# Performance work log

Hardware: AMD Instinct MI355X
Metric: run time of the kernel (lower is better)

## Reference

```python
import jax, jax.numpy as jnp
import numpy as np

NUM_GROUPS = 8   # num_groups1, recursive_index=False path
NUM_HEADS = 8


def setup_inputs() -> dict:
    key = jax.random.key(0)
    k1, k2, k3 = jax.random.split(key, 3)
    B, C, H, W = 4, 256, 64, 64
    x = jax.random.normal(k1, (B, C, H, W), dtype=jnp.float32)
    w_qkv = jax.random.normal(k2, (3 * C, C), dtype=jnp.float32) * 0.02
    w_proj = jax.random.normal(k3, (C, C), dtype=jnp.float32) * 0.02
    b_proj = jnp.zeros((C,), dtype=jnp.float32)
    return {"x": x, "w_qkv": w_qkv, "w_proj": w_proj, "b_proj": b_proj}


def reference(x, w_qkv, w_proj, b_proj):
    B, C, H, W = x.shape
    N = H * W
    G = NUM_GROUPS
    nh = NUM_HEADS
    hd = C // nh
    M = N // G
    scale = hd ** -0.5

    # b c h w -> b (h w) c
    xf = x.reshape(B, C, N).transpose(0, 2, 1)  # [B, N, C]

    # qkv linear (no bias), then split into groups / heads
    qkv = (xf @ w_qkv.T).reshape(B, G, M, 3, nh, hd)
    qkv = jnp.transpose(qkv, (3, 0, 1, 4, 2, 5))  # [3, B, G, nh, M, hd]
    q, k, v = qkv[0], qkv[1], qkv[2]

    # grouped multi-head attention, manual softmax
    attn = jax.nn.softmax(jnp.einsum('bghmd,bghnd->bghmn', q, k) * scale, axis=-1)
    out = jnp.einsum('bghmn,bghnd->bghmd', attn, v)

    # [B,G,nh,M,hd] -> [B,G,M,C] -> [B,N,C]
    out = out.transpose(0, 1, 3, 2, 4).reshape(B, N, C)

    out = out @ w_proj.T + b_proj

    # b (h w) c -> b c h w
    return out.transpose(0, 2, 1).reshape(B, C, H, W)
```

## Files before the change

### kernel.cpp

```cpp
#include <hip/hip_runtime.h>
#include <hip/hip_bf16.h>

#define Bb 4
#define Cc 256
#define Nn 4096
#define Gg 8
#define NHh 8
#define HDd 32
#define Mm 512

typedef __bf16 bf16_t;
typedef __bf16 bf16x2 __attribute__((ext_vector_type(2)));
typedef __bf16 bf16x4 __attribute__((ext_vector_type(4)));
typedef __bf16 bf16x8 __attribute__((ext_vector_type(8)));
typedef float f32x4 __attribute__((ext_vector_type(4)));

#define LSCALE (0.17677669529663687f * 1.44269504088896340f)

__device__ __forceinline__ void load_lds16(const bf16_t* g, bf16_t* l) {
  __builtin_amdgcn_global_load_lds(
      (const __attribute__((address_space(1))) void*)g,
      (__attribute__((address_space(3))) void*)l, 16, 0, 0);
}

__global__ __launch_bounds__(256) void prep_kernel(
    const float* __restrict__ x, bf16_t* __restrict__ xT,
    const float* __restrict__ wqkv, const float* __restrict__ wproj,
    bf16_t* __restrict__ wq_b, bf16_t* __restrict__ wp_b) {
  int bid = blockIdx.x, tid = threadIdx.x;
  if (bid >= 1024) {
    int i = (bid - 1024) * 256 + tid;
    wq_b[i] = (bf16_t)wqkv[i];
    if (i < Cc * Cc) wp_b[i] = (bf16_t)wproj[i];
    return;
  }
  __shared__ float t[64][65];
  int b = bid >> 8, c0 = ((bid >> 6) & 3) * 64, n0 = (bid & 63) * 64;
  const float* xp = x + ((long long)b * Cc + c0) * Nn + n0;
#pragma unroll
  for (int it = 0; it < 4; ++it) {
    int idx = it * 256 + tid;
    int r = idx >> 4, col = (idx & 15) * 4;
    f32x4 v = *(const f32x4*)&xp[(long long)r * Nn + col];
    t[r][col] = v[0];
    t[r][col + 1] = v[1];
    t[r][col + 2] = v[2];
    t[r][col + 3] = v[3];
  }
  __syncthreads();
  bf16_t* op = xT + ((long long)b * Nn + n0) * Cc + c0;
#pragma unroll
  for (int it = 0; it < 2; ++it) {
    int idx = it * 256 + tid;
    int n = idx >> 3, cg = (idx & 7) * 8;
    bf16x8 w;
#pragma unroll
    for (int j = 0; j < 8; ++j) w[j] = (bf16_t)t[cg + j][n];
    *(bf16x8*)&op[(long long)n * Cc + cg] = w;
  }
}

__global__ __launch_bounds__(256, 4) void qkv_gemm_kernel(
    const bf16_t* __restrict__ xT, const bf16_t* __restrict__ wqb,
    bf16_t* __restrict__ Qh, bf16_t* __restrict__ Kh, bf16_t* __restrict__ Vh) {
  __shared__ bf16_t smem[20480];
  int bid = blockIdx.x;
  int m0 = (bid / 3) * 64;
  int n0 = (bid % 3) * 256;
  int tid = threadIdx.x, lane = tid & 63, wid = tid >> 6;
  int quad = lane >> 4, l16 = lane & 15;
  int wn = wid * 64;

  f32x4 acc[4][4];
#pragma unroll
  for (int i = 0; i < 4; ++i)
#pragma unroll
    for (int j = 0; j < 4; ++j) acc[i][j] = (f32x4){0.f, 0.f, 0.f, 0.f};

  int scol = (lane & 3) * 8;
  int arow = lane >> 2;
  auto stage = [&](int bufi, int k0) {
    load_lds16(&xT[(long long)(m0 + wid * 16 + arow) * Cc + k0 + scol],
               &smem[bufi * 2048 + wid * 512]);
#pragma unroll
    for (int r = 0; r < 4; ++r) {
      int ch = wid * 4 + r;
      load_lds16(&wqb[(long long)(n0 + ch * 16 + arow) * Cc + k0 + scol],
                 &smem[4096 + bufi * 8192 + ch * 512]);
    }
  };

  stage(0, 0);
  __syncthreads();
  for (int t = 0; t < 8; ++t) {
    if (t < 7) stage((t + 1) & 1, (t + 1) * 32);
    const bf16_t* Ap = &smem[(t & 1) * 2048];
    const bf16_t* Bp = &smem[4096 + (t & 1) * 8192];
    bf16x8 a[4], b[4];
#pragma unroll
    for (int i = 0; i < 4; ++i)
      a[i] = *(const bf16x8*)&Ap[(i * 16 + l16) * 32 + quad * 8];
#pragma unroll
    for (int j = 0; j < 4; ++j)
      b[j] = *(const bf16x8*)&Bp[(wn + j * 16 + l16) * 32 + quad * 8];
#pragma unroll
    for (int i = 0; i < 4; ++i)
#pragma unroll
      for (int j = 0; j < 4; ++j)
        acc[i][j] = __builtin_amdgcn_mfma_f32_16x16x32_bf16(a[i], b[j], acc[i][j], 0, 0, 0);
    __syncthreads();
  }

  if (n0 < 512) {
    const bool isQ = (n0 == 0);
    const float s = isQ ? LSCALE : 1.0f;
#pragma unroll
    for (int i = 0; i < 4; ++i)
#pragma unroll
      for (int j = 0; j < 4; ++j) {
        int f = wn + j * 16 + l16;
#pragma unroll
        for (int r = 0; r < 4; ++r) {
          int lm = i * 16 + quad * 4 + r;
          smem[lm * 264 + f] = (bf16_t)(acc[i][j][r] * s);
        }
      }
    __syncthreads();
    int lm = tid >> 2, d0 = (tid & 3) * 8;
    int row = m0 + lm;
    int bb = row >> 12, gg = (row >> 9) & 7, m = row & 511;
    bf16_t* dst = isQ ? Qh : Kh;
#pragma unroll
    for (int hh = 0; hh < 8; ++hh) {
      long long hb = (long long)((bb << 6) | (gg << 3) | hh) * (Mm * HDd);
      bf16x8 w = *(bf16x8*)&smem[lm * 264 + hh * 32 + d0];
      *(bf16x8*)&dst[hb + m * HDd + d0] = w;
    }
  } else {
#pragma unroll
    for (int i = 0; i < 4; ++i) {
#pragma unroll
      for (int j = 0; j < 4; ++j) {
        int f = wn + j * 16 + l16;
        int hh = f >> 5, d = f & 31;
        int row = m0 + i * 16 + quad * 4;
        int bb = row >> 12, gg = (row >> 9) & 7, m = row & 511;
        long long hb = (long long)((bb << 6) | (gg << 3) | hh) * (Mm * HDd);
        bf16x4 w;
#pragma unroll
        for (int r = 0; r < 4; ++r) w[r] = (bf16_t)acc[i][j][r];
        *(bf16x4*)&Vh[hb + (long long)d * Mm + m] = w;
      }
    }
  }
}

__global__ __launch_bounds__(256, 4) void attn_kernel(
    const bf16_t* __restrict__ Qh, const bf16_t* __restrict__ Kh,
    const bf16_t* __restrict__ Vh, bf16_t* __restrict__ Oa) {
  __shared__ bf16_t Ks[256 * 32];
  __shared__ bf16_t Vs[32 * 264];
  int gid = blockIdx.x;
  int ms = gid & 3, head = gid >> 2;
  int h = head & 7, g = (head >> 3) & 7, b = head >> 6;
  int tid = threadIdx.x, lane = tid & 63, wid = tid >> 6;
  int quad = lane >> 4, l16 = lane & 15;

  const bf16_t* Kg = Kh + (long long)head * (Mm * HDd);
  const bf16_t* Vg = Vh + (long long)head * (Mm * HDd);
  const bf16_t* Qg = Qh + (long long)head * (Mm * HDd) + (ms * 128 + wid * 32) * HDd;

  bf16x8 qa = *(const bf16x8*)&Qg[l16 * HDd + quad * 8];
  bf16x8 qb = *(const bf16x8*)&Qg[(16 + l16) * HDd + quad * 8];

  bf16x8 ones;
#pragma unroll
  for (int i = 0; i < 8; ++i) ones[i] = (bf16_t)1.0f;

  int rp0 = ((l16 >> 2) << 3) | (l16 & 3);
  const bf16_t* Kp0 = &Ks[rp0 * HDd + quad * 8];
  const bf16_t* Kp1 = Kp0 + 4 * HDd;
  const bf16_t* VsL = &Vs[l16 * 264 + quad * 8];
  const bf16_t* VsH = &Vs[(16 + l16) * 264 + quad * 8];
  const f32x4 zero = (f32x4){0.f, 0.f, 0.f, 0.f};

  f32x4 oLa = zero, oHa = zero, oLb = zero, oHb = zero;
  f32x4 ra = zero, rb = zero;

#pragma unroll 1
  for (int ph = 0; ph < 2; ++ph) {
    __syncthreads();
#pragma unroll
    for (int it = 0; it < 4; ++it) {
      int ch = wid * 4 + it;
      load_lds16(&Kg[ph * 8192 + ch * 512 + lane * 8], &Ks[ch * 512]);
    }
#pragma unroll
    for (int i = 0; i < 4; ++i) {
      int idx = i * 256 + tid;
      int d = idx >> 5, c16 = idx & 31;
      bf16x8 v = *(const bf16x8*)&Vg[d * Mm + ph * 256 + c16 * 8];
      *(bf16x8*)&Vs[d * 264 + c16 * 8] = v;
    }
    __syncthreads();

#pragma unroll
    for (int c = 0; c < 8; ++c) {
      int nb = c * 32;
      bf16x8 kf0 = *(const bf16x8*)&Kp0[nb * HDd];
      bf16x8 kf1 = *(const bf16x8*)&Kp1[nb * HDd];
      f32x4 sa0 = __builtin_amdgcn_mfma_f32_16x16x32_bf16(kf0, qa, zero, 0, 0, 0);
      f32x4 sa1 = __builtin_amdgcn_mfma_f32_16x16x32_bf16(kf1, qa, zero, 0, 0, 0);
      f32x4 sb0 = __builtin_amdgcn_mfma_f32_16x16x32_bf16(kf0, qb, zero, 0, 0, 0);
      f32x4 sb1 = __builtin_amdgcn_mfma_f32_16x16x32_bf16(kf1, qb, zero, 0, 0, 0);
      bf16x8 pa, pb;
#pragma unroll
      for (int r = 0; r < 4; ++r) {
        pa[r] = (bf16_t)__builtin_exp2f(sa0[r]);
        pa[4 + r] = (bf16_t)__builtin_exp2f(sa1[r]);
        pb[r] = (bf16_t)__builtin_exp2f(sb0[r]);
        pb[4 + r] = (bf16_t)__builtin_exp2f(sb1[r]);
      }
      bf16x8 vL = *(const bf16x8*)&VsL[nb];
      bf16x8 vH = *(const bf16x8*)&VsH[nb];
      oLa = __builtin_amdgcn_mfma_f32_16x16x32_bf16(vL, pa, oLa, 0, 0, 0);
      oHa = __builtin_amdgcn_mfma_f32_16x16x32_bf16(vH, pa, oHa, 0, 0, 0);
      oLb = __builtin_amdgcn_mfma_f32_16x16x32_bf16(vL, pb, oLb, 0, 0, 0);
      oHb = __builtin_amdgcn_mfma_f32_16x16x32_bf16(vH, pb, oHb, 0, 0, 0);
      ra = __builtin_amdgcn_mfma_f32_16x16x32_bf16(ones, pa, ra, 0, 0, 0);
      rb = __builtin_amdgcn_mfma_f32_16x16x32_bf16(ones, pb, rb, 0, 0, 0);
    }
  }

  float inva = 1.f / ra[0], invb = 1.f / rb[0];

  long long orowa =
      ((long long)(b * Nn + g * Mm + ms * 128 + wid * 32 + l16)) * Cc + h * HDd;
  long long orowb = orowa + 16 * Cc;
  bf16x4 wLa, wHa, wLb, wHb;
#pragma unroll
  for (int r = 0; r < 4; ++r) {
    wLa[r] = (bf16_t)(oLa[r] * inva);
    wHa[r] = (bf16_t)(oHa[r] * inva);
    wLb[r] = (bf16_t)(oLb[r] * invb);
    wHb[r] = (bf16_t)(oHb[r] * invb);
  }
  *(bf16x4*)&Oa[orowa + quad * 4] = wLa;
  *(bf16x4*)&Oa[orowa + 16 + quad * 4] = wHa;
  *(bf16x4*)&Oa[orowb + quad * 4] = wLb;
  *(bf16x4*)&Oa[orowb + 16 + quad * 4] = wHb;
}

__global__ __launch_bounds__(256, 4) void proj_kernel(
    const bf16_t* __restrict__ Wp, const bf16_t* __restrict__ Oa,
    float* __restrict__ out, const float* __restrict__ bias) {
  __shared__ bf16_t As[2][64 * 32];
  __shared__ bf16_t Bs[2][64 * 32];
  int tid = threadIdx.x, lane = tid & 63, wid = tid >> 6;
  int quad = lane >> 4, l16 = lane & 15;
  int z = blockIdx.z;
  const bf16_t* Bt = Oa + (long long)z * Nn * Cc;
  int m0 = blockIdx.y * 64, n0 = blockIdx.x * 64;

  f32x4 acc[4];
#pragma unroll
  for (int i = 0; i < 4; ++i) acc[i] = (f32x4){0.f, 0.f, 0.f, 0.f};

  int scol = (lane & 3) * 8;
  int arow = lane >> 2;
  auto stage = [&](int bufi, int k0) {
    load_lds16(&Wp[(long long)(m0 + wid * 16 + arow) * Cc + k0 + scol],
               &As[bufi][wid * 512]);
    load_lds16(&Bt[(long long)(n0 + wid * 16 + arow) * Cc + k0 + scol],
               &Bs[bufi][wid * 512]);
  };

  stage(0, 0);
  __syncthreads();
  for (int t = 0; t < 8; ++t) {
    if (t < 7) stage((t + 1) & 1, (t + 1) * 32);
    const bf16_t* Ap = As[t & 1];
    const bf16_t* Bp = Bs[t & 1];
    bf16x8 a[4], b;
#pragma unroll
    for (int i = 0; i < 4; ++i)
      a[i] = *(const bf16x8*)&Ap[(i * 16 + l16) * 32 + quad * 8];
    b = *(const bf16x8*)&Bp[(wid * 16 + l16) * 32 + quad * 8];
#pragma unroll
    for (int i = 0; i < 4; ++i)
      acc[i] = __builtin_amdgcn_mfma_f32_16x16x32_bf16(a[i], b, acc[i], 0, 0, 0);
    __syncthreads();
  }

#pragma unroll
  for (int i = 0; i < 4; ++i) {
    int col = n0 + wid * 16 + l16;
#pragma unroll
    for (int r = 0; r < 4; ++r) {
      int row = m0 + i * 16 + quad * 4 + r;
      out[(long long)z * (Cc * Nn) + (long long)row * Nn + col] =
          acc[i][r] + bias[row];
    }
  }
}

extern "C" void kernel_launch(void* const* d_in, const int* in_sizes, int n_in,
                              void* d_out, int out_size, void* d_ws, size_t ws_size,
                              hipStream_t stream) {
  (void)in_sizes; (void)n_in; (void)out_size; (void)ws_size;
  const float* x = (const float*)d_in[0];
  const float* w_qkv = (const float*)d_in[1];
  const float* w_proj = (const float*)d_in[2];
  const float* b_proj = (const float*)d_in[3];
  float* out = (float*)d_out;

  char* ws = (char*)d_ws;
  bf16_t* xT  = (bf16_t*)(ws);
  bf16_t* wqb = (bf16_t*)(ws + 8388608);
  bf16_t* wpb = (bf16_t*)(ws + 8781824);
  bf16_t* Qh  = (bf16_t*)(ws + 8912896);
  bf16_t* Kh  = (bf16_t*)(ws + 17301504);
  bf16_t* Vh  = (bf16_t*)(ws + 25690112);
  bf16_t* Oa  = (bf16_t*)(ws + 34078720);

  prep_kernel<<<1792, 256, 0, stream>>>(x, xT, w_qkv, w_proj, wqb, wpb);
  qkv_gemm_kernel<<<768, 256, 0, stream>>>(xT, wqb, Qh, Kh, Vh);
  attn_kernel<<<1024, 256, 0, stream>>>(Qh, Kh, Vh, Oa);
  proj_kernel<<<dim3(64, 4, 4), 256, 0, stream>>>(wpb, Oa, out, b_proj);
}
```

Baseline: 122.4 us.

## Stage V epilogue through LDS and prefetch second V tile in attention

```diff
diff --git a/kernel.cpp b/kernel.cpp
--- a/kernel.cpp
+++ b/kernel.cpp
@@ -122,7 +122,7 @@
 #pragma unroll
         for (int r = 0; r < 4; ++r) {
           int lm = i * 16 + quad * 4 + r;
-          smem[lm * 264 + f] = (bf16_t)(acc[i][j][r] * s);
+          smem[lm * 268 + f] = (bf16_t)(acc[i][j][r] * s);
         }
       }
     __syncthreads();
@@ -133,24 +133,29 @@
 #pragma unroll
     for (int hh = 0; hh < 8; ++hh) {
       long long hb = (long long)((bb << 6) | (gg << 3) | hh) * (Mm * HDd);
-      bf16x8 w = *(bf16x8*)&smem[lm * 264 + hh * 32 + d0];
+      bf16x8 w = *(bf16x8*)&smem[lm * 268 + hh * 32 + d0];
       *(bf16x8*)&dst[hb + m * HDd + d0] = w;
     }
   } else {
 #pragma unroll
-    for (int i = 0; i < 4; ++i) {
+    for (int i = 0; i < 4; ++i)
 #pragma unroll
       for (int j = 0; j < 4; ++j) {
         int f = wn + j * 16 + l16;
-        int hh = f >> 5, d = f & 31;
-        int row = m0 + i * 16 + quad * 4;
-        int bb = row >> 12, gg = (row >> 9) & 7, m = row & 511;
-        long long hb = (long long)((bb << 6) | (gg << 3) | hh) * (Mm * HDd);
-        bf16x4 w;
-#pragma unroll
-        for (int r = 0; r < 4; ++r) w[r] = (bf16_t)acc[i][j][r];
-        *(bf16x4*)&Vh[hb + (long long)d * Mm + m] = w;
+#pragma unroll
+        for (int r = 0; r < 4; ++r)
+          smem[f * 72 + i * 16 + quad * 4 + r] = (bf16_t)acc[i][j][r];
       }
+    __syncthreads();
+    int bb = m0 >> 12, gg = (m0 >> 9) & 7, mb = m0 & 511;
+#pragma unroll
+    for (int it = 0; it < 8; ++it) {
+      int idx = it * 256 + tid;
+      int f = idx >> 3, seg = idx & 7;
+      int hh = f >> 5, d = f & 31;
+      long long hb = (long long)((bb << 6) | (gg << 3) | hh) * (Mm * HDd);
+      bf16x8 w = *(bf16x8*)&smem[f * 72 + seg * 8];
+      *(bf16x8*)&Vh[hb + (long long)d * Mm + mb + seg * 8] = w;
     }
   }
 }
@@ -187,23 +192,7 @@
   f32x4 oLa = zero, oHa = zero, oLb = zero, oHb = zero;
   f32x4 ra = zero, rb = zero;
 
-#pragma unroll 1
-  for (int ph = 0; ph < 2; ++ph) {
-    __syncthreads();
-#pragma unroll
-    for (int it = 0; it < 4; ++it) {
-      int ch = wid * 4 + it;
-      load_lds16(&Kg[ph * 8192 + ch * 512 + lane * 8], &Ks[ch * 512]);
-    }
-#pragma unroll
-    for (int i = 0; i < 4; ++i) {
-      int idx = i * 256 + tid;
-      int d = idx >> 5, c16 = idx & 31;
-      bf16x8 v = *(const bf16x8*)&Vg[d * Mm + ph * 256 + c16 * 8];
-      *(bf16x8*)&Vs[d * 264 + c16 * 8] = v;
-    }
-    __syncthreads();
-
+  auto inner = [&]() {
 #pragma unroll
     for (int c = 0; c < 8; ++c) {
       int nb = c * 32;
@@ -230,7 +219,43 @@
       ra = __builtin_amdgcn_mfma_f32_16x16x32_bf16(ones, pa, ra, 0, 0, 0);
       rb = __builtin_amdgcn_mfma_f32_16x16x32_bf16(ones, pb, rb, 0, 0, 0);
     }
-  }
+  };
+
+#pragma unroll
+  for (int it = 0; it < 4; ++it) {
+    int ch = wid * 4 + it;
+    load_lds16(&Kg[ch * 512 + lane * 8], &Ks[ch * 512]);
+  }
+  bf16x8 vcur[4], vnxt[4];
+#pragma unroll
+  for (int i = 0; i < 4; ++i) {
+    int idx = i * 256 + tid;
+    int d = idx >> 5, c16 = idx & 31;
+    vcur[i] = *(const bf16x8*)&Vg[d * Mm + c16 * 8];
+    vnxt[i] = *(const bf16x8*)&Vg[d * Mm + 256 + c16 * 8];
+  }
+#pragma unroll
+  for (int i = 0; i < 4; ++i) {
+    int idx = i * 256 + tid;
+    int d = idx >> 5, c16 = idx & 31;
+    *(bf16x8*)&Vs[d * 264 + c16 * 8] = vcur[i];
+  }
+  __syncthreads();
+  inner();
+  __syncthreads();
+#pragma unroll
+  for (int it = 0; it < 4; ++it) {
+    int ch = wid * 4 + it;
+    load_lds16(&Kg[8192 + ch * 512 + lane * 8], &Ks[ch * 512]);
+  }
+#pragma unroll
+  for (int i = 0; i < 4; ++i) {
+    int idx = i * 256 + tid;
+    int d = idx >> 5, c16 = idx & 31;
+    *(bf16x8*)&Vs[d * 264 + c16 * 8] = vnxt[i];
+  }
+  __syncthreads();
+  inner();
 
   float inva = 1.f / ra[0], invb = 1.f / rb[0];
 
```

After: 120.0 us. No clear change (-1.9%).
